# Kernel optimization log

Hardware: AMD Instinct MI355X
Metric: run time of the kernel (lower is better)

The kernel has to match this reference:

```python
import jax, jax.numpy as jnp
import numpy as np

NUM_TOKENS = 16384
MODEL_DIM = 4096
MAX_EXPERTS = 128
INITIAL_EXPERTS = 64
THRESHOLD = 0.5  # rm_threshold


def setup_inputs() -> dict:
    key = jax.random.key(0)
    k1, k2 = jax.random.split(key)
    x = jax.random.normal(k1, (NUM_TOKENS, MODEL_DIM), dtype=jnp.float32)
    # Linear(model_dim, max_expert_num, bias=False).weight -> [E_max, D]
    wg_weight = jax.random.normal(k2, (MAX_EXPERTS, MODEL_DIM), dtype=jnp.float32) * (1.0 / np.sqrt(MODEL_DIM))
    # experts_mask: first `INITIAL_EXPERTS` active
    experts_mask = (jnp.arange(MAX_EXPERTS) < INITIAL_EXPERTS).astype(jnp.float32)
    return {"x": x, "wg_weight": wg_weight, "experts_mask": experts_mask}


def reference(x, wg_weight, experts_mask):
    # gate logits: [N, E_max]
    scores = jnp.einsum("nd,ed->ne", x, wg_weight)
    # mask inactive experts
    scores = jnp.where(experts_mask[None, :] == 0, jnp.float32(-1e9), scores)
    # fp32 softmax + epsilon (matches F.softmax(..., dtype=float32) + 1e-14)
    scores = jax.nn.softmax(scores.astype(jnp.float32), axis=-1) + 1e-14
    # sort descending along expert dim
    sorted_scores = -jnp.sort(-scores, axis=-1)
    cum_scores = jnp.cumsum(sorted_scores, axis=-1)
    # adaptive top-k: experts needed to accumulate THRESHOLD routing mass
    mask = (cum_scores - sorted_scores) < THRESHOLD
    top_k = mask.sum(axis=-1).astype(jnp.int32)
    active_experts = experts_mask.sum().astype(jnp.int32)
    top_k = jnp.minimum(top_k, active_experts)
    return scores.astype(x.dtype), top_k
```

## Files before the change

### kernel.cpp

```cpp
#include <hip/hip_runtime.h>
#include <hip/hip_bf16.h>
#include <stdint.h>

#define NTOK 16384
#define DDIM 4096
#define NEXP 128
#define BM 32
#define BK 64
#define BKP 72

typedef __attribute__((ext_vector_type(8))) short short8;
typedef __attribute__((ext_vector_type(4))) float f32x4;

__device__ __forceinline__ void split_bf16(float f, uint32_t& h, uint32_t& l) {
    uint32_t u = __float_as_uint(f);
    h = (u + 0x7FFFu + ((u >> 16) & 1u)) >> 16;
    float r = f - __uint_as_float(h << 16);
    uint32_t v = __float_as_uint(r);
    l = (v + 0x7FFFu + ((v >> 16) & 1u)) >> 16;
}

__global__ void prep_w(const float* __restrict__ w,
                       uint16_t* __restrict__ whi, uint16_t* __restrict__ wlo) {
    int i = (blockIdx.x * blockDim.x + threadIdx.x) * 4;
    float4 f = *(const float4*)(w + i);
    uint32_t h0, h1, h2, h3, l0, l1, l2, l3;
    split_bf16(f.x, h0, l0);
    split_bf16(f.y, h1, l1);
    split_bf16(f.z, h2, l2);
    split_bf16(f.w, h3, l3);
    uint2 hv = make_uint2(h0 | (h1 << 16), h2 | (h3 << 16));
    uint2 lv = make_uint2(l0 | (l1 << 16), l2 | (l3 << 16));
    *(uint2*)(whi + i) = hv;
    *(uint2*)(wlo + i) = lv;
}

__global__ __launch_bounds__(256, 2) void gemm_logits(
    const float* __restrict__ x,
    const uint16_t* __restrict__ whi, const uint16_t* __restrict__ wlo,
    float* __restrict__ S)
{
    __shared__ uint16_t sAh[BM * BKP], sAl[BM * BKP];
    __shared__ uint16_t sBh[NEXP * BKP], sBl[NEXP * BKP];

    const int tid  = threadIdx.x;
    const int lane = tid & 63;
    const int wave = tid >> 6;
    const int m0   = blockIdx.x * BM;

    const int am  = tid >> 3;
    const int akc = tid & 7;
    const float* xp = x + (size_t)(m0 + am) * DDIM + akc * 8;

    f32x4 acc[2][2];
    #pragma unroll
    for (int mt = 0; mt < 2; ++mt)
        #pragma unroll
        for (int nt = 0; nt < 2; ++nt)
            acc[mt][nt] = (f32x4){0.f, 0.f, 0.f, 0.f};

    const int q = lane >> 4;
    const int c = lane & 15;

    for (int k0 = 0; k0 < DDIM; k0 += BK) {
        float4 fa = *(const float4*)(xp + k0);
        float4 fb = *(const float4*)(xp + k0 + 4);
        uint32_t h[8], l[8];
        split_bf16(fa.x, h[0], l[0]); split_bf16(fa.y, h[1], l[1]);
        split_bf16(fa.z, h[2], l[2]); split_bf16(fa.w, h[3], l[3]);
        split_bf16(fb.x, h[4], l[4]); split_bf16(fb.y, h[5], l[5]);
        split_bf16(fb.z, h[6], l[6]); split_bf16(fb.w, h[7], l[7]);
        uint4 hv = make_uint4(h[0] | (h[1] << 16), h[2] | (h[3] << 16),
                              h[4] | (h[5] << 16), h[6] | (h[7] << 16));
        uint4 lv = make_uint4(l[0] | (l[1] << 16), l[2] | (l[3] << 16),
                              l[4] | (l[5] << 16), l[6] | (l[7] << 16));
        *(uint4*)&sAh[am * BKP + akc * 8] = hv;
        *(uint4*)&sAl[am * BKP + akc * 8] = lv;

        #pragma unroll
        for (int i = 0; i < 4; ++i) {
            int ch = tid + i * 256;
            int n = ch >> 3, kc = ch & 7;
            const size_t go = (size_t)n * DDIM + k0 + kc * 8;
            uint4 bh = *(const uint4*)(whi + go);
            uint4 bl = *(const uint4*)(wlo + go);
            *(uint4*)&sBh[n * BKP + kc * 8] = bh;
            *(uint4*)&sBl[n * BKP + kc * 8] = bl;
        }
        __syncthreads();

        #pragma unroll
        for (int ks = 0; ks < 2; ++ks) {
            const int kb = ks * 32 + q * 8;
            short8 ah[2], alo[2], bh[2], blo[2];
            #pragma unroll
            for (int mt = 0; mt < 2; ++mt) {
                const int ro = (mt * 16 + c) * BKP + kb;
                ah[mt]  = *(const short8*)&sAh[ro];
                alo[mt] = *(const short8*)&sAl[ro];
            }
            #pragma unroll
            for (int nt = 0; nt < 2; ++nt) {
                const int ro = (wave * 32 + nt * 16 + c) * BKP + kb;
                bh[nt]  = *(const short8*)&sBh[ro];
                blo[nt] = *(const short8*)&sBl[ro];
            }
            #pragma unroll
            for (int mt = 0; mt < 2; ++mt)
                #pragma unroll
                for (int nt = 0; nt < 2; ++nt) {
                    acc[mt][nt] = __builtin_amdgcn_mfma_f32_16x16x32_bf16(alo[mt], bh[nt],  acc[mt][nt], 0, 0, 0);
                    acc[mt][nt] = __builtin_amdgcn_mfma_f32_16x16x32_bf16(ah[mt],  blo[nt], acc[mt][nt], 0, 0, 0);
                    acc[mt][nt] = __builtin_amdgcn_mfma_f32_16x16x32_bf16(ah[mt],  bh[nt],  acc[mt][nt], 0, 0, 0);
                }
        }
        __syncthreads();
    }

    #pragma unroll
    for (int mt = 0; mt < 2; ++mt)
        #pragma unroll
        for (int nt = 0; nt < 2; ++nt) {
            const int e = wave * 32 + nt * 16 + c;
            #pragma unroll
            for (int r = 0; r < 4; ++r) {
                const int tok = m0 + mt * 16 + q * 4 + r;
                S[(size_t)tok * NEXP + e] = acc[mt][nt][r];
            }
        }
}

__global__ __launch_bounds__(256) void postproc(
    float* __restrict__ S, const float* __restrict__ mask,
    float* __restrict__ topk_out)
{
    const int lane = threadIdx.x & 63;
    const int wave = threadIdx.x >> 6;
    const int t = blockIdx.x * 4 + wave;
    float* row = S + (size_t)t * NEXP;

    float s0 = row[lane], s1 = row[lane + 64];
    float mk0 = mask[lane], mk1 = mask[lane + 64];
    const bool a0 = (mk0 != 0.f), a1 = (mk1 != 0.f);

    float mx = fmaxf(a0 ? s0 : -3.0e38f, a1 ? s1 : -3.0e38f);
    #pragma unroll
    for (int off = 32; off; off >>= 1) mx = fmaxf(mx, __shfl_xor(mx, off));

    float p0 = a0 ? __expf(s0 - mx) : 0.f;
    float p1 = a1 ? __expf(s1 - mx) : 0.f;
    float sum = p0 + p1;
    #pragma unroll
    for (int off = 32; off; off >>= 1) sum += __shfl_xor(sum, off);

    const float inv = 1.0f / sum;
    const float sc0 = p0 * inv + 1e-14f;
    const float sc1 = p1 * inv + 1e-14f;
    row[lane]      = sc0;
    row[lane + 64] = sc1;

    const int active = __popcll(__ballot(a0)) + __popcll(__ballot(a1));

    float v0 = sc0, v1 = sc1;
    float cum = 0.f;
    int k = 0;
    while (cum < 0.5f && k < NEXP) {
        float mv = fmaxf(v0, v1);
        #pragma unroll
        for (int off = 32; off; off >>= 1) mv = fmaxf(mv, __shfl_xor(mv, off));
        cum += mv;
        ++k;
        unsigned long long b = __ballot(v0 == mv || v1 == mv);
        int first = __ffsll(b) - 1;
        if (lane == first) {
            if (v0 == mv) v0 = -1.f; else v1 = -1.f;
        }
    }
    int topk = k < active ? k : active;
    if (lane == 0) topk_out[t] = (float)topk;
}

extern "C" void kernel_launch(void* const* d_in, const int* in_sizes, int n_in,
                              void* d_out, int out_size, void* d_ws, size_t ws_size,
                              hipStream_t stream) {
    (void)in_sizes; (void)n_in; (void)out_size; (void)ws_size;
    const float* x    = (const float*)d_in[0];
    const float* w    = (const float*)d_in[1];
    const float* mask = (const float*)d_in[2];

    float* S    = (float*)d_out;
    float* topk = S + (size_t)NTOK * NEXP;

    uint16_t* whi = (uint16_t*)d_ws;
    uint16_t* wlo = whi + (size_t)NEXP * DDIM;

    hipLaunchKernelGGL(prep_w, dim3((NEXP * DDIM) / (256 * 4)), dim3(256), 0, stream,
                       w, whi, wlo);
    hipLaunchKernelGGL(gemm_logits, dim3(NTOK / BM), dim3(256), 0, stream,
                       x, whi, wlo, S);
    hipLaunchKernelGGL(postproc, dim3(NTOK / 4), dim3(256), 0, stream,
                       S, mask, topk);
}
```

Baseline: 416.3 us.

## Double-buffer GEMM tiles with direct global-to-LDS loads and XOR swizzle

The logits GEMM now uses 64-token tiles with 512 threads arranged as 2x4 waves. LDS is double-buffered so the next k-tile loads while the current one computes. Weight tiles are copied straight into LDS with global_load_lds, and an XOR swizzle replaces the old padding to avoid bank conflicts. This aims to hide global memory latency and halve how often the weight matrix is re-read per token. In exchange, LDS use roughly doubles and occupancy drops to one 512-thread block per CU.

```diff
diff --git a/kernel.cpp b/kernel.cpp
--- a/kernel.cpp
+++ b/kernel.cpp
@@ -5,12 +5,18 @@
 #define NTOK 16384
 #define DDIM 4096
 #define NEXP 128
-#define BM 32
+#define BM 64
 #define BK 64
-#define BKP 72
+#define NT (DDIM / BK)
 
 typedef __attribute__((ext_vector_type(8))) short short8;
 typedef __attribute__((ext_vector_type(4))) float f32x4;
+typedef __attribute__((address_space(1))) const uint32_t gu32;
+typedef __attribute__((address_space(3))) uint32_t lu32;
+
+__device__ __forceinline__ void gload16(const void* g, void* l) {
+    __builtin_amdgcn_global_load_lds((gu32*)g, (lu32*)l, 16, 0, 0);
+}
 
 __device__ __forceinline__ void split_bf16(float f, uint32_t& h, uint32_t& l) {
     uint32_t u = __float_as_uint(f);
@@ -35,22 +41,32 @@
     *(uint2*)(wlo + i) = lv;
 }
 
-__global__ __launch_bounds__(256, 2) void gemm_logits(
+__global__ __launch_bounds__(512, 1) void gemm_logits(
     const float* __restrict__ x,
     const uint16_t* __restrict__ whi, const uint16_t* __restrict__ wlo,
     float* __restrict__ S)
 {
-    __shared__ uint16_t sAh[BM * BKP], sAl[BM * BKP];
-    __shared__ uint16_t sBh[NEXP * BKP], sBl[NEXP * BKP];
+    __shared__ uint16_t sAh[2][BM * BK], sAl[2][BM * BK];
+    __shared__ uint16_t sBh[2][NEXP * BK], sBl[2][NEXP * BK];
 
     const int tid  = threadIdx.x;
     const int lane = tid & 63;
     const int wave = tid >> 6;
-    const int m0   = blockIdx.x * BM;
-
-    const int am  = tid >> 3;
-    const int akc = tid & 7;
-    const float* xp = x + (size_t)(m0 + am) * DDIM + akc * 8;
+    const int wr = wave >> 2;
+    const int wc = wave & 3;
+    const int q = lane >> 4;
+    const int c = lane & 15;
+    const int rxor = c & 7;
+    const int m0 = blockIdx.x * BM;
+
+    const int ar = tid >> 3, aj = tid & 7;
+    const float* xp = x + (size_t)(m0 + ar) * DDIM + aj * 8;
+    const int aoff = ar * BK + (aj ^ (ar & 7)) * 8;
+
+    const int bjj = aj ^ (ar & 7);
+    const size_t bgo0 = (size_t)ar * DDIM + bjj * 8;
+    const size_t bgo1 = bgo0 + (size_t)64 * DDIM;
+    const int bd0 = tid * 8, bd1 = (tid + 512) * 8;
 
     f32x4 acc[2][2];
     #pragma unroll
@@ -59,12 +75,17 @@
         for (int nt = 0; nt < 2; ++nt)
             acc[mt][nt] = (f32x4){0.f, 0.f, 0.f, 0.f};
 
-    const int q = lane >> 4;
-    const int c = lane & 15;
-
-    for (int k0 = 0; k0 < DDIM; k0 += BK) {
-        float4 fa = *(const float4*)(xp + k0);
-        float4 fb = *(const float4*)(xp + k0 + 4);
+    const int rA0 = (wr * 32 + c) * BK;
+    const int rB0 = (wc * 32 + c) * BK;
+
+    auto stageB = [&](int nxt, int kn) {
+        gload16(whi + bgo0 + kn, &sBh[nxt][bd0]);
+        gload16(whi + bgo1 + kn, &sBh[nxt][bd1]);
+        gload16(wlo + bgo0 + kn, &sBl[nxt][bd0]);
+        gload16(wlo + bgo1 + kn, &sBl[nxt][bd1]);
+    };
+
+    auto writeA = [&](int nxt, float4 fa, float4 fb) {
         uint32_t h[8], l[8];
         split_bf16(fa.x, h[0], l[0]); split_bf16(fa.y, h[1], l[1]);
         split_bf16(fa.z, h[2], l[2]); split_bf16(fa.w, h[3], l[3]);
@@ -74,36 +95,26 @@
                               h[4] | (h[5] << 16), h[6] | (h[7] << 16));
         uint4 lv = make_uint4(l[0] | (l[1] << 16), l[2] | (l[3] << 16),
                               l[4] | (l[5] << 16), l[6] | (l[7] << 16));
-        *(uint4*)&sAh[am * BKP + akc * 8] = hv;
-        *(uint4*)&sAl[am * BKP + akc * 8] = lv;
-
-        #pragma unroll
-        for (int i = 0; i < 4; ++i) {
-            int ch = tid + i * 256;
-            int n = ch >> 3, kc = ch & 7;
-            const size_t go = (size_t)n * DDIM + k0 + kc * 8;
-            uint4 bh = *(const uint4*)(whi + go);
-            uint4 bl = *(const uint4*)(wlo + go);
-            *(uint4*)&sBh[n * BKP + kc * 8] = bh;
-            *(uint4*)&sBl[n * BKP + kc * 8] = bl;
-        }
-        __syncthreads();
-
+        *(uint4*)&sAh[nxt][aoff] = hv;
+        *(uint4*)&sAl[nxt][aoff] = lv;
+    };
+
+    auto compute = [&](int cur) {
         #pragma unroll
         for (int ks = 0; ks < 2; ++ks) {
-            const int kb = ks * 32 + q * 8;
+            const int off = ((((ks << 2) | q)) ^ rxor) << 3;
             short8 ah[2], alo[2], bh[2], blo[2];
             #pragma unroll
             for (int mt = 0; mt < 2; ++mt) {
-                const int ro = (mt * 16 + c) * BKP + kb;
-                ah[mt]  = *(const short8*)&sAh[ro];
-                alo[mt] = *(const short8*)&sAl[ro];
+                const int ro = rA0 + mt * 16 * BK + off;
+                ah[mt]  = *(const short8*)&sAh[cur][ro];
+                alo[mt] = *(const short8*)&sAl[cur][ro];
             }
             #pragma unroll
             for (int nt = 0; nt < 2; ++nt) {
-                const int ro = (wave * 32 + nt * 16 + c) * BKP + kb;
-                bh[nt]  = *(const short8*)&sBh[ro];
-                blo[nt] = *(const short8*)&sBl[ro];
+                const int ro = rB0 + nt * 16 * BK + off;
+                bh[nt]  = *(const short8*)&sBh[cur][ro];
+                blo[nt] = *(const short8*)&sBl[cur][ro];
             }
             #pragma unroll
             for (int mt = 0; mt < 2; ++mt)
@@ -114,17 +125,37 @@
                     acc[mt][nt] = __builtin_amdgcn_mfma_f32_16x16x32_bf16(ah[mt],  bh[nt],  acc[mt][nt], 0, 0, 0);
                 }
         }
+    };
+
+    stageB(0, 0);
+    {
+        float4 fa = *(const float4*)(xp);
+        float4 fb = *(const float4*)(xp + 4);
+        writeA(0, fa, fb);
+    }
+    __syncthreads();
+
+    #pragma unroll 2
+    for (int t = 0; t < NT - 1; ++t) {
+        const int cur = t & 1, nxt = cur ^ 1;
+        const int kn = (t + 1) * BK;
+        stageB(nxt, kn);
+        float4 fa = *(const float4*)(xp + kn);
+        float4 fb = *(const float4*)(xp + kn + 4);
+        compute(cur);
+        writeA(nxt, fa, fb);
         __syncthreads();
     }
+    compute((NT - 1) & 1);
 
     #pragma unroll
     for (int mt = 0; mt < 2; ++mt)
         #pragma unroll
         for (int nt = 0; nt < 2; ++nt) {
-            const int e = wave * 32 + nt * 16 + c;
+            const int e = wc * 32 + nt * 16 + c;
             #pragma unroll
             for (int r = 0; r < 4; ++r) {
-                const int tok = m0 + mt * 16 + q * 4 + r;
+                const int tok = m0 + wr * 32 + mt * 16 + q * 4 + r;
                 S[(size_t)tok * NEXP + e] = acc[mt][nt][r];
             }
         }
@@ -196,7 +227,7 @@
 
     hipLaunchKernelGGL(prep_w, dim3((NEXP * DDIM) / (256 * 4)), dim3(256), 0, stream,
                        w, whi, wlo);
-    hipLaunchKernelGGL(gemm_logits, dim3(NTOK / BM), dim3(256), 0, stream,
+    hipLaunchKernelGGL(gemm_logits, dim3(NTOK / BM), dim3(512), 0, stream,
                        x, whi, wlo, S);
     hipLaunchKernelGGL(postproc, dim3(NTOK / 4), dim3(256), 0, stream,
                        S, mask, topk);
```

Result: no change. 421.2 us (+1.2%).
